# Optimization experiments

Measured on AMD Instinct MI355X. Metric: run time of the kernel, lower is better.

## Reference

```python
import jax, jax.numpy as jnp
import numpy as np


def setup_inputs() -> dict:
    key = jax.random.key(0)
    ks = jax.random.split(key, 6)
    B, L, NC = 32, 10000, 80
    REG_MAX, K, HID = 32, 4, 64
    IN = 4 * (K + 1)  # 20
    scores = jax.random.normal(ks[0], (B, L, NC), dtype=jnp.float32)
    pred_corners = jax.random.normal(ks[1], (B, L, 4 * (REG_MAX + 1)), dtype=jnp.float32)
    w1 = jax.random.normal(ks[2], (HID, IN), dtype=jnp.float32) * (1.0 / np.sqrt(IN))
    b1 = jax.random.normal(ks[3], (HID,), dtype=jnp.float32) * 0.01
    w2 = jax.random.normal(ks[4], (1, HID), dtype=jnp.float32) * (1.0 / np.sqrt(HID))
    b2 = jax.random.normal(ks[5], (1,), dtype=jnp.float32) * 0.01
    return {"scores": scores, "pred_corners": pred_corners,
            "w1": w1, "b1": b1, "w2": w2, "b2": b2, "k_top": K}


def reference(scores, pred_corners, w1, b1, w2, b2, k_top):
    B, L, D = pred_corners.shape
    nbins = D // 4  # reg_max + 1
    # softmax over the distribution bins of each of the 4 box sides
    prob = jax.nn.softmax(pred_corners.reshape(B, L, 4, nbins), axis=-1)
    prob_topk, _ = jax.lax.top_k(prob, k_top)                      # [B, L, 4, k]
    stat = jnp.concatenate(
        [prob_topk, prob_topk.mean(axis=-1, keepdims=True)], axis=-1)  # [B, L, 4, k+1]
    stat = stat.reshape(B, L, 4 * (k_top + 1))                     # [B, L, 4*(k+1)]
    # tiny MLP: Linear -> ReLU -> Linear
    h = jax.nn.relu(jnp.einsum('bli,hi->blh', stat, w1) + b1)      # [B, L, hid]
    quality = jnp.einsum('blh,oh->blo', h, w2) + b2                # [B, L, 1]
    return scores + quality
```

## Files before the change

kernel.cpp:

```cpp
#include <hip/hip_runtime.h>
#include <cmath>


constexpr int NB   = 33;
constexpr int DPR  = 132;
constexpr int HID  = 64;
constexpr int NCLS = 80;
constexpr int APB  = 256;

__global__
__attribute__((amdgpu_flat_work_group_size(APB, APB), amdgpu_waves_per_eu(4, 5)))
void lqe_fused(
    const float* __restrict__ scores,
    const float* __restrict__ pred,
    const float* __restrict__ w1,
    const float* __restrict__ b1,
    const float* __restrict__ w2,
    const float* __restrict__ b2,
    float* __restrict__ out)
{
    __shared__ float s_w1[HID * 16];
    __shared__ float s_b1[HID];
    __shared__ float s_w2[HID];
    __shared__ float s_b2;
    __shared__ float s_q[APB];

    const int t = threadIdx.x;
    const long long ab = (long long)blockIdx.x * APB;

    for (int i = t; i < HID * 16; i += APB) {
        int j = i >> 4, col = i & 15;
        int s = col >> 2, q = col & 3;
        s_w1[i] = w1[j * 20 + s * 5 + q] + 0.25f * w1[j * 20 + s * 5 + 4];
    }
    if (t < HID) { s_b1[t] = b1[t]; s_w2[t] = w2[t]; }
    if (t == 0)  { s_b2 = b2[0]; }
    __syncthreads();

    const float4* pp = (const float4*)(pred + (ab + t) * (long long)DPR);

    float f[16];
    float e0 = 0.f, e1 = 0.f, e2 = 0.f, e3 = 0.f, sum = 0.f;

    #pragma unroll
    for (int b = 0; b < 3; ++b) {
        float4 buf[11];
        #pragma unroll
        for (int ld = 0; ld < 11; ++ld) buf[ld] = pp[b * 11 + ld];
        #pragma unroll
        for (int ld = 0; ld < 11; ++ld) {
            float vv[4] = {buf[ld].x, buf[ld].y, buf[ld].z, buf[ld].w};
            #pragma unroll
            for (int c = 0; c < 4; ++c) {
                const int idx = b * 44 + 4 * ld + c;
                float e = __expf(vv[c]);
                sum += e;
                float n0 = fminf(e0, e);  e0 = fmaxf(e0, e);
                float n1 = fminf(e1, n0); e1 = fmaxf(e1, n0);
                float n2 = fminf(e2, n1); e2 = fmaxf(e2, n1);
                e3 = fmaxf(e3, n2);
                if (idx % NB == NB - 1) {
                    const int s = idx / NB;
                    float inv = 1.0f / sum;
                    f[s * 4 + 0] = e0 * inv;
                    f[s * 4 + 1] = e1 * inv;
                    f[s * 4 + 2] = e2 * inv;
                    f[s * 4 + 3] = e3 * inv;
                    e0 = e1 = e2 = e3 = 0.f; sum = 0.f;
                }
            }
        }
    }

    float qv = s_b2;
    #pragma unroll
    for (int j = 0; j < HID; ++j) {
        const float4* wr = (const float4*)(s_w1 + j * 16);
        float hj = s_b1[j];
        #pragma unroll
        for (int i4 = 0; i4 < 4; ++i4) {
            float4 w = wr[i4];
            hj = fmaf(f[4 * i4 + 0], w.x, hj);
            hj = fmaf(f[4 * i4 + 1], w.y, hj);
            hj = fmaf(f[4 * i4 + 2], w.z, hj);
            hj = fmaf(f[4 * i4 + 3], w.w, hj);
        }
        hj = fmaxf(hj, 0.f);
        qv = fmaf(hj, s_w2[j], qv);
    }

    s_q[t] = qv;
    __syncthreads();

    const float4* sc4 = (const float4*)(scores + ab * NCLS);
    float4*       ot4 = (float4*)(out + ab * NCLS);
    #pragma unroll 1
    for (int i = t; i < APB * NCLS / 4; i += APB) {
        float q = s_q[i / 20];
        float4 v = sc4[i];
        v.x += q; v.y += q; v.z += q; v.w += q;
        ot4[i] = v;
    }
}

extern "C" void kernel_launch(void* const* d_in, const int* in_sizes, int n_in,
                              void* d_out, int out_size, void* d_ws, size_t ws_size,
                              hipStream_t stream) {
    const float* scores = (const float*)d_in[0];
    const float* pred   = (const float*)d_in[1];
    const float* w1     = (const float*)d_in[2];
    const float* b1     = (const float*)d_in[3];
    const float* w2     = (const float*)d_in[4];
    const float* b2     = (const float*)d_in[5];

    int n_anchor = in_sizes[0] / NCLS;
    int blocks   = n_anchor / APB;
    lqe_fused<<<blocks, APB, 0, stream>>>(scores, pred, w1, b1, w2, b2,
                                          (float*)d_out);
}
```

Measured before the change: 346.3 us.

## Stage pred rows into LDS via direct global-to-LDS DMA with smaller blocks

Shrinks the block to 64 anchors and copies each block's prediction rows into shared memory with global_load_lds 16-byte transfers, so the global reads are coalesced instead of each thread striding across its own 528-byte row. The softmax/top-k pass then reads its row from LDS. The scores epilogue is fully unrolled so all 20 float4 loads are issued before any store. In exchange it uses about 34KB of LDS per block, which can limit occupancy, and the w1 preload now assumes APB equals HID.

Result: no change. 348.6 us (+0.7%).

```diff
diff --git a/kernel.cpp b/kernel.cpp
--- a/kernel.cpp
+++ b/kernel.cpp
@@ -1,4 +1,5 @@
 #include <hip/hip_runtime.h>
+#include <cstdint>
 #include <cmath>
 
 
@@ -6,10 +7,18 @@
 constexpr int DPR  = 132;
 constexpr int HID  = 64;
 constexpr int NCLS = 80;
-constexpr int APB  = 256;
+constexpr int APB  = 64;
+
+#define AS_GLOBAL __attribute__((address_space(1)))
+#define AS_LDS    __attribute__((address_space(3)))
+
+__device__ __forceinline__ void dma16(const void* g, void* l) {
+    __builtin_amdgcn_global_load_lds((const AS_GLOBAL uint32_t*)g,
+                                     (AS_LDS uint32_t*)l, 16, 0, 0);
+}
 
 __global__
-__attribute__((amdgpu_flat_work_group_size(APB, APB), amdgpu_waves_per_eu(4, 5)))
+__attribute__((amdgpu_flat_work_group_size(APB, APB), amdgpu_waves_per_eu(1, 4)))
 void lqe_fused(
     const float* __restrict__ scores,
     const float* __restrict__ pred,
@@ -19,6 +28,7 @@
     const float* __restrict__ b2,
     float* __restrict__ out)
 {
+    __shared__ float s_pred[APB * DPR];
     __shared__ float s_w1[HID * 16];
     __shared__ float s_b1[HID];
     __shared__ float s_w2[HID];
@@ -28,46 +38,56 @@
     const int t = threadIdx.x;
     const long long ab = (long long)blockIdx.x * APB;
 
-    for (int i = t; i < HID * 16; i += APB) {
-        int j = i >> 4, col = i & 15;
-        int s = col >> 2, q = col & 3;
-        s_w1[i] = w1[j * 20 + s * 5 + q] + 0.25f * w1[j * 20 + s * 5 + 4];
+    {
+        const uint32_t* g = (const uint32_t*)pred + ab * DPR;
+        uint32_t* l = (uint32_t*)s_pred;
+        #pragma unroll
+        for (int k = 0; k < 33; ++k)
+            dma16(g + k * 256 + t * 4,
+                  l + k * 256);
     }
-    if (t < HID) { s_b1[t] = b1[t]; s_w2[t] = w2[t]; }
-    if (t == 0)  { s_b2 = b2[0]; }
+
+    {
+        #pragma unroll
+        for (int s = 0; s < 4; ++s) {
+            float wm = 0.25f * w1[t * 20 + s * 5 + 4];
+            #pragma unroll
+            for (int q = 0; q < 4; ++q)
+                s_w1[t * 16 + s * 4 + q] = w1[t * 20 + s * 5 + q] + wm;
+        }
+        s_b1[t] = b1[t];
+        s_w2[t] = w2[t];
+        if (t == 0) s_b2 = b2[0];
+    }
+
     __syncthreads();
 
-    const float4* pp = (const float4*)(pred + (ab + t) * (long long)DPR);
+    const float4* lp = (const float4*)(s_pred + t * DPR);
 
     float f[16];
     float e0 = 0.f, e1 = 0.f, e2 = 0.f, e3 = 0.f, sum = 0.f;
 
     #pragma unroll
-    for (int b = 0; b < 3; ++b) {
-        float4 buf[11];
+    for (int ld = 0; ld < 33; ++ld) {
+        float4 v4 = lp[ld];
+        float vv[4] = {v4.x, v4.y, v4.z, v4.w};
         #pragma unroll
-        for (int ld = 0; ld < 11; ++ld) buf[ld] = pp[b * 11 + ld];
-        #pragma unroll
-        for (int ld = 0; ld < 11; ++ld) {
-            float vv[4] = {buf[ld].x, buf[ld].y, buf[ld].z, buf[ld].w};
-            #pragma unroll
-            for (int c = 0; c < 4; ++c) {
-                const int idx = b * 44 + 4 * ld + c;
-                float e = __expf(vv[c]);
-                sum += e;
-                float n0 = fminf(e0, e);  e0 = fmaxf(e0, e);
-                float n1 = fminf(e1, n0); e1 = fmaxf(e1, n0);
-                float n2 = fminf(e2, n1); e2 = fmaxf(e2, n1);
-                e3 = fmaxf(e3, n2);
-                if (idx % NB == NB - 1) {
-                    const int s = idx / NB;
-                    float inv = 1.0f / sum;
-                    f[s * 4 + 0] = e0 * inv;
-                    f[s * 4 + 1] = e1 * inv;
-                    f[s * 4 + 2] = e2 * inv;
-                    f[s * 4 + 3] = e3 * inv;
-                    e0 = e1 = e2 = e3 = 0.f; sum = 0.f;
-                }
+        for (int c = 0; c < 4; ++c) {
+            const int idx = 4 * ld + c;
+            float e = __expf(vv[c]);
+            sum += e;
+            float n0 = fminf(e0, e);  e0 = fmaxf(e0, e);
+            float n1 = fminf(e1, n0); e1 = fmaxf(e1, n0);
+            float n2 = fminf(e2, n1); e2 = fmaxf(e2, n1);
+            e3 = fmaxf(e3, n2);
+            if (idx % NB == NB - 1) {
+                const int s = idx / NB;
+                float inv = 1.0f / sum;
+                f[s * 4 + 0] = e0 * inv;
+                f[s * 4 + 1] = e1 * inv;
+                f[s * 4 + 2] = e2 * inv;
+                f[s * 4 + 3] = e3 * inv;
+                e0 = e1 = e2 = e3 = 0.f; sum = 0.f;
             }
         }
     }
@@ -94,12 +114,21 @@
 
     const float4* sc4 = (const float4*)(scores + ab * NCLS);
     float4*       ot4 = (float4*)(out + ab * NCLS);
-    #pragma unroll 1
-    for (int i = t; i < APB * NCLS / 4; i += APB) {
-        float q = s_q[i / 20];
-        float4 v = sc4[i];
-        v.x += q; v.y += q; v.z += q; v.w += q;
-        ot4[i] = v;
+
+    float4 v[20];
+    float  q[20];
+    #pragma unroll
+    for (int u = 0; u < 20; ++u) {
+        const int i = u * APB + t;
+        v[u] = sc4[i];
+        q[u] = s_q[i / 20];
+    }
+    #pragma unroll
+    for (int u = 0; u < 20; ++u) {
+        const int i = u * APB + t;
+        float4 w = v[u];
+        w.x += q[u]; w.y += q[u]; w.z += q[u]; w.w += q[u];
+        ot4[i] = w;
     }
 }
 
```

## Split into quality and add kernels with inline-asm rolling prefetch of pred rows

Applied to the files above, without the earlier changes.

Splits the fused kernel into two. The first computes per-anchor quality using an 8-deep rolling register buffer of hand-issued global_load_dwordx4 with explicit vmcnt waits, so loads overlap the softmax/top-k work. The second is a flat elementwise kernel that adds the quality to scores. This removes the block-level barrier and the serialized score pass inside the fused kernel, and raises occupancy. In exchange it adds a second launch and a workspace round trip for q. The asm waits rely on exact load counts, so any compiler-inserted loads could break the vmcnt accounting.

New measurement: 375.4 us. 8.4% more time.

```diff
diff --git a/kernel.cpp b/kernel.cpp
--- a/kernel.cpp
+++ b/kernel.cpp
@@ -1,4 +1,5 @@
 #include <hip/hip_runtime.h>
+#include <cstdint>
 #include <cmath>
 
 
@@ -6,73 +7,93 @@
 constexpr int DPR  = 132;
 constexpr int HID  = 64;
 constexpr int NCLS = 80;
-constexpr int APB  = 256;
 
-__global__
-__attribute__((amdgpu_flat_work_group_size(APB, APB), amdgpu_waves_per_eu(4, 5)))
-void lqe_fused(
-    const float* __restrict__ scores,
+struct QState {
+    float e0, e1, e2, e3, sum;
+    float f[16];
+};
+
+template<int K>
+__device__ __forceinline__ void qstep(float4 (&buf)[8], uint64_t addr, QState& st)
+{
+    constexpr int NWAIT = (K < 25) ? 7 : (32 - K);
+    asm volatile("s_waitcnt vmcnt(%0)" :: "n"(NWAIT) : "memory");
+    __builtin_amdgcn_sched_barrier(0);
+    float4 v4 = buf[K & 7];
+    float vv[4] = {v4.x, v4.y, v4.z, v4.w};
+    #pragma unroll
+    for (int c = 0; c < 4; ++c) {
+        const int idx = 4 * K + c;
+        float e = __expf(vv[c]);
+        st.sum += e;
+        float n0 = fminf(st.e0, e);  st.e0 = fmaxf(st.e0, e);
+        float n1 = fminf(st.e1, n0); st.e1 = fmaxf(st.e1, n0);
+        float n2 = fminf(st.e2, n1); st.e2 = fmaxf(st.e2, n1);
+        st.e3 = fmaxf(st.e3, n2);
+        if (idx % NB == NB - 1) {
+            const int s = idx / NB;
+            float inv = 1.0f / st.sum;
+            st.f[s * 4 + 0] = st.e0 * inv;
+            st.f[s * 4 + 1] = st.e1 * inv;
+            st.f[s * 4 + 2] = st.e2 * inv;
+            st.f[s * 4 + 3] = st.e3 * inv;
+            st.e0 = st.e1 = st.e2 = st.e3 = 0.f; st.sum = 0.f;
+        }
+    }
+    if constexpr (K + 8 < 33) {
+        asm volatile("global_load_dwordx4 %0, %1, off offset:%2"
+                     : "=v"(buf[K & 7]) : "v"(addr), "n"(16 * (K + 8)));
+    }
+}
+
+template<int K>
+__device__ __forceinline__ void qsteps(float4 (&buf)[8], uint64_t addr, QState& st)
+{
+    qstep<K>(buf, addr, st);
+    if constexpr (K < 32) qsteps<K + 1>(buf, addr, st);
+}
+
+template<int K>
+__device__ __forceinline__ void qprime(float4 (&buf)[8], uint64_t addr)
+{
+    asm volatile("global_load_dwordx4 %0, %1, off offset:%2"
+                 : "=v"(buf[K]) : "v"(addr), "n"(16 * K));
+    if constexpr (K < 7) qprime<K + 1>(buf, addr);
+}
+
+__global__ __launch_bounds__(256, 5)
+void lqe_q(
     const float* __restrict__ pred,
     const float* __restrict__ w1,
     const float* __restrict__ b1,
     const float* __restrict__ w2,
     const float* __restrict__ b2,
-    float* __restrict__ out)
+    float* __restrict__ qout)
 {
     __shared__ float s_w1[HID * 16];
     __shared__ float s_b1[HID];
     __shared__ float s_w2[HID];
-    __shared__ float s_b2;
-    __shared__ float s_q[APB];
 
     const int t = threadIdx.x;
-    const long long ab = (long long)blockIdx.x * APB;
-
-    for (int i = t; i < HID * 16; i += APB) {
-        int j = i >> 4, col = i & 15;
-        int s = col >> 2, q = col & 3;
+    const float b2r = b2[0];
+    for (int i = t; i < HID * 16; i += 256) {
+        int j = i >> 4, col = i & 15, s = col >> 2, q = col & 3;
         s_w1[i] = w1[j * 20 + s * 5 + q] + 0.25f * w1[j * 20 + s * 5 + 4];
     }
     if (t < HID) { s_b1[t] = b1[t]; s_w2[t] = w2[t]; }
-    if (t == 0)  { s_b2 = b2[0]; }
     __syncthreads();
 
-    const float4* pp = (const float4*)(pred + (ab + t) * (long long)DPR);
+    const long long a = (long long)blockIdx.x * 256 + t;
+    const uint64_t addr = (uint64_t)(pred + a * (long long)DPR);
 
-    float f[16];
-    float e0 = 0.f, e1 = 0.f, e2 = 0.f, e3 = 0.f, sum = 0.f;
+    float4 buf[8];
+    qprime<0>(buf, addr);
 
-    #pragma unroll
-    for (int b = 0; b < 3; ++b) {
-        float4 buf[11];
-        #pragma unroll
-        for (int ld = 0; ld < 11; ++ld) buf[ld] = pp[b * 11 + ld];
-        #pragma unroll
-        for (int ld = 0; ld < 11; ++ld) {
-            float vv[4] = {buf[ld].x, buf[ld].y, buf[ld].z, buf[ld].w};
-            #pragma unroll
-            for (int c = 0; c < 4; ++c) {
-                const int idx = b * 44 + 4 * ld + c;
-                float e = __expf(vv[c]);
-                sum += e;
-                float n0 = fminf(e0, e);  e0 = fmaxf(e0, e);
-                float n1 = fminf(e1, n0); e1 = fmaxf(e1, n0);
-                float n2 = fminf(e2, n1); e2 = fmaxf(e2, n1);
-                e3 = fmaxf(e3, n2);
-                if (idx % NB == NB - 1) {
-                    const int s = idx / NB;
-                    float inv = 1.0f / sum;
-                    f[s * 4 + 0] = e0 * inv;
-                    f[s * 4 + 1] = e1 * inv;
-                    f[s * 4 + 2] = e2 * inv;
-                    f[s * 4 + 3] = e3 * inv;
-                    e0 = e1 = e2 = e3 = 0.f; sum = 0.f;
-                }
-            }
-        }
-    }
+    QState st;
+    st.e0 = st.e1 = st.e2 = st.e3 = st.sum = 0.f;
+    qsteps<0>(buf, addr, st);
 
-    float qv = s_b2;
+    float qv = b2r;
     #pragma unroll
     for (int j = 0; j < HID; ++j) {
         const float4* wr = (const float4*)(s_w1 + j * 16);
@@ -80,27 +101,28 @@
         #pragma unroll
         for (int i4 = 0; i4 < 4; ++i4) {
             float4 w = wr[i4];
-            hj = fmaf(f[4 * i4 + 0], w.x, hj);
-            hj = fmaf(f[4 * i4 + 1], w.y, hj);
-            hj = fmaf(f[4 * i4 + 2], w.z, hj);
-            hj = fmaf(f[4 * i4 + 3], w.w, hj);
+            hj = fmaf(st.f[4 * i4 + 0], w.x, hj);
+            hj = fmaf(st.f[4 * i4 + 1], w.y, hj);
+            hj = fmaf(st.f[4 * i4 + 2], w.z, hj);
+            hj = fmaf(st.f[4 * i4 + 3], w.w, hj);
         }
         hj = fmaxf(hj, 0.f);
         qv = fmaf(hj, s_w2[j], qv);
     }
+    qout[a] = qv;
+}
 
-    s_q[t] = qv;
-    __syncthreads();
-
-    const float4* sc4 = (const float4*)(scores + ab * NCLS);
-    float4*       ot4 = (float4*)(out + ab * NCLS);
-    #pragma unroll 1
-    for (int i = t; i < APB * NCLS / 4; i += APB) {
-        float q = s_q[i / 20];
-        float4 v = sc4[i];
-        v.x += q; v.y += q; v.z += q; v.w += q;
-        ot4[i] = v;
-    }
+__global__ __launch_bounds__(256)
+void lqe_add(
+    const float* __restrict__ scores,
+    const float* __restrict__ qin,
+    float* __restrict__ out)
+{
+    const int i = blockIdx.x * 256 + threadIdx.x;
+    const float q = qin[i / 20];
+    float4 v = ((const float4*)scores)[i];
+    v.x += q; v.y += q; v.z += q; v.w += q;
+    ((float4*)out)[i] = v;
 }
 
 extern "C" void kernel_launch(void* const* d_in, const int* in_sizes, int n_in,
@@ -114,7 +136,10 @@
     const float* b2     = (const float*)d_in[5];
 
     int n_anchor = in_sizes[0] / NCLS;
-    int blocks   = n_anchor / APB;
-    lqe_fused<<<blocks, APB, 0, stream>>>(scores, pred, w1, b1, w2, b2,
-                                          (float*)d_out);
+    float* qbuf  = (float*)d_ws;
+
+    lqe_q<<<n_anchor / 256, 256, 0, stream>>>(pred, w1, b1, w2, b2, qbuf);
+
+    int nf4 = n_anchor * (NCLS / 4);
+    lqe_add<<<nf4 / 256, 256, 0, stream>>>(scores, qbuf, (float*)d_out);
 }
```
